# Performance work log

Hardware: AMD Instinct MI355X
Metric: run time of the kernel (lower is better)

Reference implementation:

```python
import jax, jax.numpy as jnp
import numpy as np

B, S, T, C = 8, 25, 75, 5  # tasks, support per task, targets per task, classes per set
CAP = S // C               # fixed slot capacity used by the torch scatter buffer
EPS = 1e-8


def _conv(x, W, b):
    # x: [N, Cin, H, W], W: [Cout, Cin, 3, 3] (OIHW), stride 2, SAME padding
    y = jax.lax.conv_general_dilated(
        x, W, window_strides=(2, 2), padding='SAME',
        dimension_numbers=('NCHW', 'OIHW', 'NCHW'))
    return jax.nn.relu(y + b[None, :, None, None])


def _encode(x, W1, b1, W2, b2, W3, b3, W4, b4):
    # Conv4 backbone: 84 -> 42 -> 21 -> 11 -> 6 spatial, 64 channels
    x = _conv(x, W1, b1)
    x = _conv(x, W2, b2)
    x = _conv(x, W3, b3)
    x = _conv(x, W4, b4)
    return x.reshape(x.shape[0], -1)  # [N, 2304]


def setup_inputs() -> dict:
    key = jax.random.key(0)
    ks = jax.random.split(key, 8)
    inp = {
        'x_support_set': jax.random.normal(ks[0], (B, S, 3, 84, 84), jnp.float32),
        'x_target_set': jax.random.normal(ks[1], (B, T, 3, 84, 84), jnp.float32),
        # arange labels -> y % C is perfectly class-balanced per task (CAP each)
        'y_support_set': jnp.arange(B * S, dtype=jnp.int32).reshape(B, S),
        'W1': jax.random.normal(ks[2], (64, 3, 3, 3), jnp.float32) * 0.1,
        'b1': jnp.zeros((64,), jnp.float32),
        'W2': jax.random.normal(ks[3], (64, 64, 3, 3), jnp.float32) * 0.05,
        'b2': jnp.zeros((64,), jnp.float32),
        'W3': jax.random.normal(ks[4], (64, 64, 3, 3), jnp.float32) * 0.05,
        'b3': jnp.zeros((64,), jnp.float32),
        'W4': jax.random.normal(ks[5], (64, 64, 3, 3), jnp.float32) * 0.05,
        'b4': jnp.zeros((64,), jnp.float32),
    }
    return inp


def reference(x_support_set, x_target_set, y_support_set,
              W1, b1, W2, b2, W3, b3, W4, b4):
    # Encode support set: [B*S, 3, 84, 84] -> [B, S, D]
    emb_s = _encode(x_support_set.reshape(-1, 3, 84, 84),
                    W1, b1, W2, b2, W3, b3, W4, b4).reshape(B, S, -1)
    # Per-class prototypes: torch builds a zero buffer [C, CAP, D], scatters each
    # embedding into slot (y % C), then .mean(1). With balanced labels that is a
    # segment-sum over classes divided by the fixed capacity CAP.
    onehot = jax.nn.one_hot(y_support_set % C, C, dtype=emb_s.dtype)  # [B, S, C]
    protos = jnp.einsum('bsc,bsd->bcd', onehot, emb_s) / CAP          # [B, C, D]
    # Encode target set: [B, T, D]
    emb_t = _encode(x_target_set.reshape(-1, 3, 84, 84),
                    W1, b1, W2, b2, W3, b3, W4, b4).reshape(B, T, -1)
    # Cosine-similarity logits (matching-network classification head)
    tn = emb_t / jnp.maximum(jnp.linalg.norm(emb_t, axis=-1, keepdims=True), EPS)
    pn = protos / jnp.maximum(jnp.linalg.norm(protos, axis=-1, keepdims=True), EPS)
    preds = jnp.einsum('btd,bcd->btc', tn, pn)  # [B, T, C]
    return preds
```

## Files before the change

### kernel.cpp

```cpp
#include <hip/hip_runtime.h>
#include <hip/hip_bf16.h>


#define BB 8
#define SS 25
#define TT 75
#define CC 5
#define DD 2304
#define NSUP 200
#define NTGT 600
#define NTOT 800
#define EPSF 1e-8f

typedef __attribute__((ext_vector_type(8))) short bf16x8;
typedef __attribute__((ext_vector_type(4))) float f32x4;

__device__ __forceinline__ float load_ext(const void* p, size_t idx, int isf32) {
  if (isf32) return ((const float*)p)[idx];
  unsigned short u = ((const unsigned short*)p)[idx];
  union { unsigned int i; float f; } v;
  v.i = ((unsigned int)u) << 16;
  return v.f;
}

__global__ void fsc_probe_dtype_k(const unsigned short* __restrict__ w2raw,
                                  int nelems, int* __restrict__ flag) {
  __shared__ int cnt;
  if (threadIdx.x == 0) cnt = 0;
  __syncthreads();
  int local = 0;
  for (int i = threadIdx.x; i < nelems; i += 256) {
    unsigned short u = w2raw[i];
    int ex = (u >> 7) & 0xFF;
    if (ex != 0 && (ex < 0x69 || ex > 0x84)) local++;
  }
  atomicAdd(&cnt, local);
  __syncthreads();
  if (threadIdx.x == 0) *flag = (cnt > nelems / 8) ? 1 : 0;
}

__global__ void fsc_repack_w1m_k(const void* __restrict__ W,
                                 __hip_bfloat16* __restrict__ Wf,
                                 const int* __restrict__ flag) {
  const int isf32 = *flag;
  int i = blockIdx.x * blockDim.x + threadIdx.x;
  if (i >= 4096) return;
  int j = i & 7;
  int lane = (i >> 3) & 63;
  int t = (i >> 9) & 3;
  int s = i >> 11;
  int kk = (lane >> 4) * 8 + j;
  int co = t * 16 + (lane & 15);
  float v = 0.f;
  int kh, kwp, ci;
  bool live = false;
  if (s == 0) { kh = kk >> 4; kwp = (kk & 15) >> 2; ci = kk & 3; live = true; }
  else if (kk < 16) { kh = 2; kwp = kk >> 2; ci = kk & 3; live = true; }
  if (live && kwp < 3 && ci < 3)
    v = load_ext(W, (size_t)((co * 3 + ci) * 3 + kh) * 3 + kwp, isf32);
  Wf[i] = __float2bfloat16(v);
}

__global__ void fsc_repack_wm_k(const void* __restrict__ W,
                                __hip_bfloat16* __restrict__ Wf,
                                const int* __restrict__ flag) {
  const int isf32 = *flag;
  int o = blockIdx.x * blockDim.x + threadIdx.x;
  if (o >= 36864) return;
  int j = o & 7;
  int lane = (o >> 3) & 63;
  int t = (o >> 9) & 3;
  int kk = o >> 11;
  int s = kk & 1;
  int khw = kk >> 1;
  int kh = khw / 3, kw = khw - kh * 3;
  int co = t * 16 + (lane & 15);
  int ci = s * 32 + (lane >> 4) * 8 + j;
  float v = load_ext(W, (size_t)((co * 64 + ci) * 3 + kh) * 3 + kw, isf32);
  Wf[o] = __float2bfloat16(v);
}

template <int P>
__global__ void fsc_zero_border_k(__hip_bfloat16* __restrict__ buf, int N) {
  int i = blockIdx.x * blockDim.x + threadIdx.x;
  const int RP = 4 * P - 4;
  if (i >= N * RP * 64) return;
  int c = i & 63;
  int r = (i >> 6) % RP;
  int n = (i >> 6) / RP;
  int row, colp;
  if (r < P) { row = 0; colp = r; }
  else if (r < 2 * P) { row = P - 1; colp = r - P; }
  else if (r < 3 * P - 2) { row = r - 2 * P + 1; colp = 0; }
  else { row = r - (3 * P - 2) + 1; colp = P - 1; }
  buf[(((size_t)n * P + row) * P + colp) * 64 + c] = __float2bfloat16(0.f);
}

__global__ void fsc_zero_xb_k(__hip_bfloat16* __restrict__ X, int N) {
  int i = blockIdx.x * blockDim.x + threadIdx.x;
  if (i >= N * 1360) return;
  int c = i & 3;
  int p = (i >> 2) % 340;
  int n = (i >> 2) / 340;
  int h, w;
  if (p < 172) { h = 84 + (p / 86); w = p % 86; }
  else { int pp = p - 172; h = pp >> 1; w = 84 + (pp & 1); }
  X[(((size_t)n * 86 + h) * 86 + w) * 4 + c] = __float2bfloat16(0.f);
}

__global__ void fsc_xform1_k(const void* __restrict__ x, int srcImg0,
                             __hip_bfloat16* __restrict__ X, int dstImg0,
                             int n, const int* __restrict__ flag) {
  const int isf32 = *flag;
  int i = blockIdx.x * blockDim.x + threadIdx.x;
  const int imgL = i / 7056;
  if (imgL >= n) return;
  const int sp = i - imgL * 7056;
  const int h = sp / 84, w = sp - h * 84;
  const size_t base = (size_t)(srcImg0 + imgL) * 21168;
  union { unsigned short u[4]; uint2 q; } pk;
#pragma unroll
  for (int ci = 0; ci < 3; ++ci)
    pk.u[ci] = __bfloat16_as_ushort(__float2bfloat16(load_ext(x, base + ci * 7056 + sp, isf32)));
  pk.u[3] = 0;
  *(uint2*)(void*)(X + (((size_t)(dstImg0 + imgL) * 86 + h) * 86 + w) * 4) = pk.q;
}

__global__ void fsc_conv1m_k(const __hip_bfloat16* __restrict__ X,
                             const __hip_bfloat16* __restrict__ Wf,
                             const void* __restrict__ bias,
                             __hip_bfloat16* __restrict__ out, int N,
                             const int* __restrict__ flag) {
  constexpr int TPI = 28;
  const int wid = blockIdx.x * 4 + (threadIdx.x >> 6);
  const int img = wid / TPI;
  if (img >= N) return;
  const int tl = wid - img * TPI;
  const int lane = threadIdx.x & 63;
  const int nidx = lane & 15, quad = lane >> 4;

  int col[4];
  bool val[4];
  int hoA[4], woA[4];
#pragma unroll
  for (int p = 0; p < 4; ++p) {
    col[p] = tl * 64 + p * 16 + nidx;
    val[p] = col[p] < 1764;
    if (!val[p]) col[p] = 1763;
    hoA[p] = col[p] / 42;
    woA[p] = col[p] - hoA[p] * 42;
  }

  f32x4 acc[4][4];
#pragma unroll
  for (int p = 0; p < 4; ++p)
#pragma unroll
    for (int t = 0; t < 4; ++t) acc[p][t] = (f32x4){0.f, 0.f, 0.f, 0.f};

#pragma unroll
  for (int s = 0; s < 2; ++s) {
    bf16x8 b[4];
#pragma unroll
    for (int p = 0; p < 4; ++p) {
      const int hi = 2 * hoA[p] + (s == 0 ? (quad >> 1) : 2);
      const __hip_bfloat16* bp =
          X + (((size_t)img * 86 + hi) * 86 + 2 * woA[p]) * 4 + (quad & 1) * 8;
      b[p] = *(const bf16x8*)(const void*)bp;
    }
#pragma unroll
    for (int t = 0; t < 4; ++t) {
      bf16x8 a = *(const bf16x8*)(const void*)(Wf + ((size_t)(s * 4 + t) * 64 + lane) * 8);
#pragma unroll
      for (int p = 0; p < 4; ++p)
        acc[p][t] = __builtin_amdgcn_mfma_f32_16x16x32_bf16(a, b[p], acc[p][t], 0, 0, 0);
    }
  }

  const int isf32 = *flag;
#pragma unroll
  for (int p = 0; p < 4; ++p) {
#pragma unroll
    for (int t = 0; t < 4; ++t) {
      float v[4];
#pragma unroll
      for (int r = 0; r < 4; ++r) {
        const int cout = t * 16 + quad * 4 + r;
        float xv = acc[p][t][r] + load_ext(bias, cout, isf32);
        v[r] = xv > 0.f ? xv : 0.f;
      }
      if (val[p]) {
        __hip_bfloat16* o = out + (((size_t)img * 44 + (hoA[p] + 1)) * 44 +
                                   (woA[p] + 1)) * 64 + t * 16 + quad * 4;
        union { unsigned short u[4]; uint2 w; } pk;
#pragma unroll
        for (int r = 0; r < 4; ++r) pk.u[r] = __bfloat16_as_ushort(__float2bfloat16(v[r]));
        *(uint2*)(void*)o = pk.w;
      }
    }
  }
}

template <int HO, int PWI, int PWO, int ROFF, int CG>
__global__ void fsc_convp_k(const __hip_bfloat16* __restrict__ in,
                            const __hip_bfloat16* __restrict__ Wf,
                            const void* __restrict__ bias,
                            __hip_bfloat16* __restrict__ out, int N,
                            const int* __restrict__ flag) {
  constexpr int COLS = CG * 16;
  constexpr int TPI = (HO * HO + COLS - 1) / COLS;
  const int wid = blockIdx.x * 4 + (threadIdx.x >> 6);
  const int img = wid / TPI;
  if (img >= N) return;
  const int tl = wid - img * TPI;
  const int lane = threadIdx.x & 63;
  const int nidx = lane & 15, quad = lane >> 4;

  int col[CG];
  bool val[CG];
  int hoA[CG], woA[CG];
  const __hip_bfloat16* bsrc[CG];
#pragma unroll
  for (int p = 0; p < CG; ++p) {
    col[p] = tl * COLS + p * 16 + nidx;
    val[p] = col[p] < HO * HO;
    if (!val[p]) col[p] = HO * HO - 1;
    hoA[p] = col[p] / HO;
    woA[p] = col[p] - hoA[p] * HO;
    bsrc[p] = in + (((size_t)img * PWI + (2 * hoA[p] + ROFF)) * PWI +
                    (2 * woA[p] + ROFF)) * 64 + quad * 8;
  }
  const __hip_bfloat16* asrc = Wf + lane * 8;

  f32x4 acc[CG][4];
#pragma unroll
  for (int p = 0; p < CG; ++p)
#pragma unroll
    for (int t = 0; t < 4; ++t) acc[p][t] = (f32x4){0.f, 0.f, 0.f, 0.f};

#define FSC_BOFF(kk) ((((kk) >> 1) / 3 * PWI + ((kk) >> 1) % 3) * 64 + ((kk)&1) * 32)

  bf16x8 bbuf[4][CG];
#pragma unroll
  for (int d = 0; d < 3; ++d)
#pragma unroll
    for (int p = 0; p < CG; ++p)
      bbuf[d][p] = *(const bf16x8*)(const void*)(bsrc[p] + FSC_BOFF(d));

#pragma unroll
  for (int kk = 0; kk < 18; ++kk) {
    if (kk + 3 < 18) {
#pragma unroll
      for (int p = 0; p < CG; ++p)
        bbuf[(kk + 3) & 3][p] =
            *(const bf16x8*)(const void*)(bsrc[p] + FSC_BOFF(kk + 3));
    }
#pragma unroll
    for (int t = 0; t < 4; ++t) {
      bf16x8 a = *(const bf16x8*)(const void*)(asrc + (kk * 4 + t) * 512);
#pragma unroll
      for (int p = 0; p < CG; ++p)
        acc[p][t] =
            __builtin_amdgcn_mfma_f32_16x16x32_bf16(a, bbuf[kk & 3][p], acc[p][t], 0, 0, 0);
    }
  }
#undef FSC_BOFF

  const int isf32 = *flag;
#pragma unroll
  for (int p = 0; p < CG; ++p) {
#pragma unroll
    for (int t = 0; t < 4; ++t) {
      float v[4];
#pragma unroll
      for (int r = 0; r < 4; ++r) {
        const int cout = t * 16 + quad * 4 + r;
        float xv = acc[p][t][r] + load_ext(bias, cout, isf32);
        v[r] = xv > 0.f ? xv : 0.f;
      }
      if (val[p]) {
        __hip_bfloat16* o = out + (((size_t)img * PWO + (hoA[p] + 1)) * PWO +
                                   (woA[p] + 1)) * 64 + t * 16 + quad * 4;
        union { unsigned short u[4]; uint2 w; } pk;
#pragma unroll
        for (int r = 0; r < 4; ++r) pk.u[r] = __bfloat16_as_ushort(__float2bfloat16(v[r]));
        *(uint2*)(void*)o = pk.w;
      }
    }
  }
}

__global__ void fsc_conv4_k(const __hip_bfloat16* __restrict__ in,
                            const __hip_bfloat16* __restrict__ Wf,
                            const void* __restrict__ bias, float* __restrict__ emb,
                            int N, const int* __restrict__ flag) {
  constexpr int HO = 6, PWI = 13;
  constexpr int TPI = 2;
  const int wid = blockIdx.x * 4 + (threadIdx.x >> 6);
  const int img = wid / TPI;
  if (img >= N) return;
  const int tl = wid - img * TPI;
  const int lane = threadIdx.x & 63;
  const int nidx = lane & 15, quad = lane >> 4;

  int col0 = tl * 32 + nidx;
  int col1 = col0 + 16;
  const bool val0 = col0 < HO * HO;
  const bool val1 = col1 < HO * HO;
  if (!val0) col0 = HO * HO - 1;
  if (!val1) col1 = HO * HO - 1;
  const int ho0 = col0 / HO, wo0 = col0 - ho0 * HO;
  const int ho1 = col1 / HO, wo1 = col1 - ho1 * HO;

  const __hip_bfloat16* bsrc0 =
      in + (((size_t)img * PWI + 2 * ho0) * PWI + 2 * wo0) * 64 + quad * 8;
  const __hip_bfloat16* bsrc1 =
      in + (((size_t)img * PWI + 2 * ho1) * PWI + 2 * wo1) * 64 + quad * 8;
  const __hip_bfloat16* asrc = Wf + lane * 8;

  f32x4 acc[2][4];
#pragma unroll
  for (int p = 0; p < 2; ++p)
#pragma unroll
    for (int t = 0; t < 4; ++t) acc[p][t] = (f32x4){0.f, 0.f, 0.f, 0.f};

#pragma unroll
  for (int kk = 0; kk < 18; ++kk) {
    const int s = kk & 1;
    const int khw = kk >> 1;
    const int kh = khw / 3, kw = khw - kh * 3;
    const int boff = (kh * PWI + kw) * 64 + s * 32;
    bf16x8 b0 = *(const bf16x8*)(const void*)(bsrc0 + boff);
    bf16x8 b1 = *(const bf16x8*)(const void*)(bsrc1 + boff);
#pragma unroll
    for (int t = 0; t < 4; ++t) {
      bf16x8 a = *(const bf16x8*)(const void*)(asrc + (kk * 4 + t) * 512);
      acc[0][t] = __builtin_amdgcn_mfma_f32_16x16x32_bf16(a, b0, acc[0][t], 0, 0, 0);
      acc[1][t] = __builtin_amdgcn_mfma_f32_16x16x32_bf16(a, b1, acc[1][t], 0, 0, 0);
    }
  }

  const int isf32 = *flag;
#pragma unroll
  for (int p = 0; p < 2; ++p) {
    const bool valid = p == 0 ? val0 : val1;
    const int col = p == 0 ? col0 : col1;
#pragma unroll
    for (int t = 0; t < 4; ++t) {
      float v[4];
#pragma unroll
      for (int r = 0; r < 4; ++r) {
        const int cout = t * 16 + quad * 4 + r;
        float xv = acc[p][t][r] + load_ext(bias, cout, isf32);
        v[r] = xv > 0.f ? xv : 0.f;
      }
      if (valid) {
        float* o = emb + ((size_t)img * 36 + col) * 64 + t * 16 + quad * 4;
        *(f32x4*)(void*)o = (f32x4){v[0], v[1], v[2], v[3]};
      }
    }
  }
}

__global__ void fsc_proto_k(const float* __restrict__ emb_s, const int* __restrict__ y,
                            float* __restrict__ protos) {
  int i = blockIdx.x * blockDim.x + threadIdx.x;
  if (i >= BB * CC * DD) return;
  int d = i % DD;
  int bc = i / DD;
  int c = bc % CC;
  int b = bc / CC;
  float sum = 0.f;
  for (int s = 0; s < SS; ++s) {
    if (y[b * SS + s] % CC == c) sum += emb_s[(size_t)(b * SS + s) * DD + d];
  }
  protos[i] = sum * 0.2f;
}

__global__ void fsc_pnorm_k(const float* __restrict__ protos, float* __restrict__ pn) {
  __shared__ float red[4];
  __shared__ float inv;
  const int bc = blockIdx.x;
  const float* p = protos + (size_t)bc * DD;
  float ss = 0.f;
  for (int d = threadIdx.x; d < DD; d += 256) { float v = p[d]; ss += v * v; }
#pragma unroll
  for (int off = 32; off > 0; off >>= 1) ss += __shfl_down(ss, off);
  if ((threadIdx.x & 63) == 0) red[threadIdx.x >> 6] = ss;
  __syncthreads();
  if (threadIdx.x == 0) {
    float nrm = sqrtf(red[0] + red[1] + red[2] + red[3]);
    nrm = nrm > EPSF ? nrm : EPSF;
    inv = 1.f / nrm;
  }
  __syncthreads();
  float sc = inv;
  for (int d = threadIdx.x; d < DD; d += 256) pn[(size_t)bc * DD + d] = p[d] * sc;
}

__global__ void fsc_preds_k(const float* __restrict__ emb_t, const float* __restrict__ pn,
                            void* __restrict__ out, const int* __restrict__ flag) {
  __shared__ float red[4][6];
  __shared__ float fin[6];
  const int isf32 = *flag;
  const int bt = blockIdx.x;
  const int b = bt / TT;
  const float* et = emb_t + (size_t)bt * DD;
  float e[9];
#pragma unroll
  for (int k = 0; k < 9; ++k) e[k] = et[threadIdx.x + 256 * k];
  float vals[6];
  {
    float ss = 0.f;
#pragma unroll
    for (int k = 0; k < 9; ++k) ss += e[k] * e[k];
    vals[0] = ss;
  }
  const float* pb = pn + (size_t)b * CC * DD;
#pragma unroll
  for (int c = 0; c < CC; ++c) {
    float s = 0.f;
#pragma unroll
    for (int k = 0; k < 9; ++k) s += e[k] * pb[(size_t)c * DD + threadIdx.x + 256 * k];
    vals[1 + c] = s;
  }
#pragma unroll
  for (int v = 0; v < 6; ++v) {
#pragma unroll
    for (int off = 32; off > 0; off >>= 1) vals[v] += __shfl_down(vals[v], off);
  }
  if ((threadIdx.x & 63) == 0) {
#pragma unroll
    for (int v = 0; v < 6; ++v) red[threadIdx.x >> 6][v] = vals[v];
  }
  __syncthreads();
  if (threadIdx.x < 6)
    fin[threadIdx.x] = red[0][threadIdx.x] + red[1][threadIdx.x] +
                       red[2][threadIdx.x] + red[3][threadIdx.x];
  __syncthreads();
  if (threadIdx.x < CC) {
    float nt = sqrtf(fin[0]);
    nt = nt > EPSF ? nt : EPSF;
    float r = fin[1 + threadIdx.x] / nt;
    if (isf32) ((float*)out)[(size_t)bt * CC + threadIdx.x] = r;
    else ((__hip_bfloat16*)out)[(size_t)bt * CC + threadIdx.x] = __float2bfloat16(r);
  }
}

static inline int fsc_cdiv(int a, int b) { return (a + b - 1) / b; }
static inline int imin(int a, int b) { return a < b ? a : b; }
static inline int imax(int a, int b) { return a > b ? a : b; }

extern "C" void kernel_launch(void* const* d_in, const int* in_sizes, int n_in,
                              void* d_out, int out_size, void* d_ws, size_t ws_size,
                              hipStream_t stream) {
  const void* xs = d_in[0];
  const void* xt = d_in[1];
  const int* y = (const int*)d_in[2];
  const void* W1 = d_in[3];
  const void* b1 = d_in[4];
  const void* W2 = d_in[5];
  const void* b2 = d_in[6];
  const void* W3 = d_in[7];
  const void* b3 = d_in[8];
  const void* W4 = d_in[9];
  const void* b4 = d_in[10];

  char* w = (char*)d_ws;
  int* flag = (int*)w;                      w += 256;
  __hip_bfloat16* Wf1 = (__hip_bfloat16*)w; w += 4096 * 2;
  __hip_bfloat16* Wf2 = (__hip_bfloat16*)w; w += 36864 * 2;
  __hip_bfloat16* Wf3 = (__hip_bfloat16*)w; w += 36864 * 2;
  __hip_bfloat16* Wf4 = (__hip_bfloat16*)w; w += 36864 * 2;
  float* protos = (float*)w;                w += (size_t)BB * CC * DD * 4;
  float* pn = (float*)w;                    w += (size_t)BB * CC * DD * 4;
  float* emb = (float*)w;                   w += (size_t)NTOT * DD * 4;
  __hip_bfloat16* C3 = (__hip_bfloat16*)w;  w += (size_t)NTOT * 13 * 13 * 64 * 2;
  char* chunk0 = w;
  const size_t fixedB = (size_t)(w - (char*)d_ws);
  const size_t szX  = (size_t)86 * 86 * 4 * 2;
  const size_t szA1 = (size_t)44 * 44 * 64 * 2;
  const size_t szA2 = (size_t)23 * 23 * 64 * 2;
  const size_t perImgB = szX + szA1 + szA2;

  int CH = 50;
  const int cands[7] = {640, 600, 512, 400, 200, 100, 50};
  for (int k = 0; k < 7; ++k) {
    if (fixedB + (size_t)cands[k] * perImgB <= ws_size) { CH = cands[k]; break; }
  }
  __hip_bfloat16* X  = (__hip_bfloat16*)chunk0;
  __hip_bfloat16* A1 = (__hip_bfloat16*)(chunk0 + (size_t)CH * szX);
  __hip_bfloat16* A2 = (__hip_bfloat16*)(chunk0 + (size_t)CH * (szX + szA1));

  fsc_probe_dtype_k<<<1, 256, 0, stream>>>((const unsigned short*)W2, 64 * 64 * 9, flag);
  fsc_repack_w1m_k<<<fsc_cdiv(4096, 256), 256, 0, stream>>>(W1, Wf1, flag);
  fsc_repack_wm_k<<<fsc_cdiv(36864, 256), 256, 0, stream>>>(W2, Wf2, flag);
  fsc_repack_wm_k<<<fsc_cdiv(36864, 256), 256, 0, stream>>>(W3, Wf3, flag);
  fsc_repack_wm_k<<<fsc_cdiv(36864, 256), 256, 0, stream>>>(W4, Wf4, flag);

  fsc_zero_xb_k<<<fsc_cdiv(CH * 1360, 256), 256, 0, stream>>>(X, CH);
  fsc_zero_border_k<44><<<fsc_cdiv(CH * (4 * 44 - 4) * 64, 256), 256, 0, stream>>>(A1, CH);
  fsc_zero_border_k<23><<<fsc_cdiv(CH * (4 * 23 - 4) * 64, 256), 256, 0, stream>>>(A2, CH);
  fsc_zero_border_k<13><<<fsc_cdiv(NTOT * (4 * 13 - 4) * 64, 256), 256, 0, stream>>>(C3, NTOT);

  for (int g0 = 0; g0 < NTOT; g0 += CH) {
    const int n = imin(CH, NTOT - g0);
    if (g0 < NSUP) {
      const int cnt = imin(g0 + n, NSUP) - g0;
      fsc_xform1_k<<<fsc_cdiv(cnt * 7056, 256), 256, 0, stream>>>(
          xs, g0, X, 0, cnt, flag);
    }
    if (g0 + n > NSUP) {
      const int tStart = imax(g0, NSUP);
      const int cnt = g0 + n - tStart;
      fsc_xform1_k<<<fsc_cdiv(cnt * 7056, 256), 256, 0, stream>>>(
          xt, tStart - NSUP, X, tStart - g0, cnt, flag);
    }
    fsc_conv1m_k<<<fsc_cdiv(n * 28, 4), 256, 0, stream>>>(X, Wf1, b1, A1, n, flag);
    fsc_convp_k<21, 44, 23, 1, 2><<<fsc_cdiv(n * 14, 4), 256, 0, stream>>>(
        A1, Wf2, b2, A2, n, flag);
    fsc_convp_k<11, 23, 13, 0, 1><<<fsc_cdiv(n * 8, 4), 256, 0, stream>>>(
        A2, Wf3, b3, C3 + (size_t)g0 * 13 * 13 * 64, n, flag);
  }

  fsc_conv4_k<<<fsc_cdiv(NTOT * 2, 4), 256, 0, stream>>>(C3, Wf4, b4, emb, NTOT, flag);

  fsc_proto_k<<<fsc_cdiv(BB * CC * DD, 256), 256, 0, stream>>>(emb, y, protos);
  fsc_pnorm_k<<<BB * CC, 256, 0, stream>>>(protos, pn);
  fsc_preds_k<<<NTGT, 256, 0, stream>>>(emb + (size_t)NSUP * DD, pn, d_out, flag);
}
```

Measured before the change: 445.9 us.

## Store conv1 output in channel-planar parity-split layout for conv2 gathers

Conv1 now writes its activation as 16 planes (8-channel groups times column parity) of 44x22, instead of NHWC 44x44x64. A dedicated conv2 kernel reads the stride-2 taps from these planes with fixed offsets and keeps a 3-deep software prefetch of B fragments. The aim is more contiguous, coalesced loads for the stride-2 conv and less address arithmetic. It also needs a new border-zeroing kernel for the padded layout and changes the A1 buffer size.

```diff
diff --git a/kernel.cpp b/kernel.cpp
--- a/kernel.cpp
+++ b/kernel.cpp
@@ -11,6 +11,9 @@
 #define NTGT 600
 #define NTOT 800
 #define EPSF 1e-8f
+
+#define PLE 7744
+#define IMG1E 123904
 
 typedef __attribute__((ext_vector_type(8))) short bf16x8;
 typedef __attribute__((ext_vector_type(4))) float f32x4;
@@ -96,6 +99,21 @@
   buf[(((size_t)n * P + row) * P + colp) * 64 + c] = __float2bfloat16(0.f);
 }
 
+__global__ void fsc_zero_a1p_k(__hip_bfloat16* __restrict__ A1, int N) {
+  int i = blockIdx.x * blockDim.x + threadIdx.x;
+  if (i >= N * 16 * 86 * 8) return;
+  int ch = i & 7;
+  int q = (i >> 3) % 86;
+  int pl = ((i >> 3) / 86) % 16;
+  int n = (i >> 3) / (86 * 16);
+  const int wp = pl & 1;
+  int h, w2;
+  if (q < 22) { h = 0; w2 = q; }
+  else if (q < 44) { h = 43; w2 = q - 22; }
+  else { h = q - 43; w2 = wp ? 21 : 0; }
+  A1[(size_t)n * IMG1E + pl * PLE + (h * 22 + w2) * 8 + ch] = __float2bfloat16(0.f);
+}
+
 __global__ void fsc_zero_xb_k(__hip_bfloat16* __restrict__ X, int N) {
   int i = blockIdx.x * blockDim.x + threadIdx.x;
   if (i >= N * 1360) return;
@@ -179,6 +197,9 @@
   const int isf32 = *flag;
 #pragma unroll
   for (int p = 0; p < 4; ++p) {
+    const int h = hoA[p] + 1;
+    const int wq = woA[p] + 1;
+    const int wp = wq & 1, w2 = wq >> 1;
 #pragma unroll
     for (int t = 0; t < 4; ++t) {
       float v[4];
@@ -189,7 +210,97 @@
         v[r] = xv > 0.f ? xv : 0.f;
       }
       if (val[p]) {
-        __hip_bfloat16* o = out + (((size_t)img * 44 + (hoA[p] + 1)) * 44 +
+        __hip_bfloat16* o = out + (size_t)img * IMG1E +
+                            ((2 * t + (quad >> 1)) * 2 + wp) * PLE +
+                            (h * 22 + w2) * 8 + (quad & 1) * 4;
+        union { unsigned short u[4]; uint2 w; } pk;
+#pragma unroll
+        for (int r = 0; r < 4; ++r) pk.u[r] = __bfloat16_as_ushort(__float2bfloat16(v[r]));
+        *(uint2*)(void*)o = pk.w;
+      }
+    }
+  }
+}
+
+__global__ void fsc_conv2p_k(const __hip_bfloat16* __restrict__ A1,
+                             const __hip_bfloat16* __restrict__ Wf,
+                             const void* __restrict__ bias,
+                             __hip_bfloat16* __restrict__ out, int N,
+                             const int* __restrict__ flag) {
+  constexpr int TPI = 14;
+  const int wid = blockIdx.x * 4 + (threadIdx.x >> 6);
+  const int img = wid / TPI;
+  if (img >= N) return;
+  const int tl = wid - img * TPI;
+  const int lane = threadIdx.x & 63;
+  const int nidx = lane & 15, quad = lane >> 4;
+
+  int col[2];
+  bool val[2];
+  int hoA[2], woA[2];
+  const __hip_bfloat16* bsrc[2];
+#pragma unroll
+  for (int p = 0; p < 2; ++p) {
+    col[p] = tl * 32 + p * 16 + nidx;
+    val[p] = col[p] < 441;
+    if (!val[p]) col[p] = 440;
+    hoA[p] = col[p] / 21;
+    woA[p] = col[p] - hoA[p] * 21;
+    bsrc[p] = A1 + (size_t)img * IMG1E + quad * (2 * PLE) +
+              ((2 * hoA[p] + 1) * 22 + woA[p]) * 8;
+  }
+  const __hip_bfloat16* asrc = Wf + lane * 8;
+
+  f32x4 acc[2][4];
+#pragma unroll
+  for (int p = 0; p < 2; ++p)
+#pragma unroll
+    for (int t = 0; t < 4; ++t) acc[p][t] = (f32x4){0.f, 0.f, 0.f, 0.f};
+
+#define FSC_BOFF2(kk)                                                        \
+  ((((kk)&1) * 8 + ((1 + (((kk) >> 1) % 3)) & 1)) * PLE +                    \
+   (((((kk) >> 1)) / 3) * 22 + ((1 + (((kk) >> 1) % 3)) >> 1)) * 8)
+
+  bf16x8 bbuf[4][2];
+#pragma unroll
+  for (int d = 0; d < 3; ++d)
+#pragma unroll
+    for (int p = 0; p < 2; ++p)
+      bbuf[d][p] = *(const bf16x8*)(const void*)(bsrc[p] + FSC_BOFF2(d));
+
+#pragma unroll
+  for (int kk = 0; kk < 18; ++kk) {
+    if (kk + 3 < 18) {
+#pragma unroll
+      for (int p = 0; p < 2; ++p)
+        bbuf[(kk + 3) & 3][p] =
+            *(const bf16x8*)(const void*)(bsrc[p] + FSC_BOFF2(kk + 3));
+    }
+#pragma unroll
+    for (int t = 0; t < 4; ++t) {
+      bf16x8 a = *(const bf16x8*)(const void*)(asrc + (kk * 4 + t) * 512);
+#pragma unroll
+      for (int p = 0; p < 2; ++p)
+        acc[p][t] =
+            __builtin_amdgcn_mfma_f32_16x16x32_bf16(a, bbuf[kk & 3][p], acc[p][t], 0, 0, 0);
+    }
+  }
+#undef FSC_BOFF2
+
+  const int isf32 = *flag;
+#pragma unroll
+  for (int p = 0; p < 2; ++p) {
+#pragma unroll
+    for (int t = 0; t < 4; ++t) {
+      float v[4];
+#pragma unroll
+      for (int r = 0; r < 4; ++r) {
+        const int cout = t * 16 + quad * 4 + r;
+        float xv = acc[p][t][r] + load_ext(bias, cout, isf32);
+        v[r] = xv > 0.f ? xv : 0.f;
+      }
+      if (val[p]) {
+        __hip_bfloat16* o = out + (((size_t)img * 23 + (hoA[p] + 1)) * 23 +
                                    (woA[p] + 1)) * 64 + t * 16 + quad * 4;
         union { unsigned short u[4]; uint2 w; } pk;
 #pragma unroll
@@ -478,7 +589,7 @@
   char* chunk0 = w;
   const size_t fixedB = (size_t)(w - (char*)d_ws);
   const size_t szX  = (size_t)86 * 86 * 4 * 2;
-  const size_t szA1 = (size_t)44 * 44 * 64 * 2;
+  const size_t szA1 = (size_t)IMG1E * 2;
   const size_t szA2 = (size_t)23 * 23 * 64 * 2;
   const size_t perImgB = szX + szA1 + szA2;
 
@@ -498,7 +609,7 @@
   fsc_repack_wm_k<<<fsc_cdiv(36864, 256), 256, 0, stream>>>(W4, Wf4, flag);
 
   fsc_zero_xb_k<<<fsc_cdiv(CH * 1360, 256), 256, 0, stream>>>(X, CH);
-  fsc_zero_border_k<44><<<fsc_cdiv(CH * (4 * 44 - 4) * 64, 256), 256, 0, stream>>>(A1, CH);
+  fsc_zero_a1p_k<<<fsc_cdiv(CH * 16 * 86 * 8, 256), 256, 0, stream>>>(A1, CH);
   fsc_zero_border_k<23><<<fsc_cdiv(CH * (4 * 23 - 4) * 64, 256), 256, 0, stream>>>(A2, CH);
   fsc_zero_border_k<13><<<fsc_cdiv(NTOT * (4 * 13 - 4) * 64, 256), 256, 0, stream>>>(C3, NTOT);
 
@@ -516,8 +627,7 @@
           xt, tStart - NSUP, X, tStart - g0, cnt, flag);
     }
     fsc_conv1m_k<<<fsc_cdiv(n * 28, 4), 256, 0, stream>>>(X, Wf1, b1, A1, n, flag);
-    fsc_convp_k<21, 44, 23, 1, 2><<<fsc_cdiv(n * 14, 4), 256, 0, stream>>>(
-        A1, Wf2, b2, A2, n, flag);
+    fsc_conv2p_k<<<fsc_cdiv(n * 14, 4), 256, 0, stream>>>(A1, Wf2, b2, A2, n, flag);
     fsc_convp_k<11, 23, 13, 0, 1><<<fsc_cdiv(n * 8, 4), 256, 0, stream>>>(
         A2, Wf3, b3, C3 + (size_t)g0 * 13 * 13 * 64, n, flag);
   }
```

Result: faster. 429.6 us (-3.7%).
